# Performance work log

Hardware: AMD Instinct MI355X
Metric: run time of the kernel (lower is better)

Reference implementation:

```python
import jax, jax.numpy as jnp
import numpy as np

EPS = 1e-5
HEADS = 4
C = 128
GROUPS = 32  # min(32, 128//4)
SR = 2
SCALE = (C // HEADS) ** -0.5


def group_norm(x, gamma, beta, groups=GROUPS, eps=EPS):
    N, Ch, H, W = x.shape
    xg = x.reshape(N, groups, Ch // groups, H, W)
    mu = xg.mean(axis=(2, 3, 4), keepdims=True)
    var = xg.var(axis=(2, 3, 4), keepdims=True)
    xg = (xg - mu) * jax.lax.rsqrt(var + eps)
    x = xg.reshape(N, Ch, H, W)
    return x * gamma[None, :, None, None] + beta[None, :, None, None]


def conv1x1(x, W, b):
    # x: [N,C,H,W], W: [Cout,Cin], b: [Cout]
    return jnp.einsum('nchw,oc->nohw', x, W) + b[None, :, None, None]


def avg_pool2(x):
    N, Ch, H, W = x.shape
    return x.reshape(N, Ch, H // SR, SR, W // SR, SR).mean(axis=(3, 5))


def to_heads(x):
    # [N,C,H,W] -> [N,h,HW,C//h]  (matches view(N,h,C/h,HW).permute(0,1,3,2))
    N, Ch, H, W = x.shape
    return x.reshape(N, HEADS, Ch // HEADS, H * W).transpose(0, 1, 3, 2)


def setup_inputs() -> dict:
    key = jax.random.key(0)
    ks = jax.random.split(key, 16)
    B, H, W = 8, 64, 64
    s = 1.0 / np.sqrt(C)
    inp = {
        'q_src': jax.random.normal(ks[0], (B, C, H, W), jnp.float32),
        'k_src': jax.random.normal(ks[1], (B, C, H, W), jnp.float32),
        'v_src': jax.random.normal(ks[2], (B, C, H, W), jnp.float32),
        'Wq': jax.random.normal(ks[3], (C, C), jnp.float32) * s,
        'bq': jnp.zeros((C,), jnp.float32),
        'Wk': jax.random.normal(ks[4], (C, C), jnp.float32) * s,
        'bk': jnp.zeros((C,), jnp.float32),
        'Wv': jax.random.normal(ks[5], (C, C), jnp.float32) * s,
        'bv': jnp.zeros((C,), jnp.float32),
        'Wp': jax.random.normal(ks[6], (C, C), jnp.float32) * s,
        'bp': jnp.zeros((C,), jnp.float32),
        'g_nq': jnp.ones((C,), jnp.float32), 'b_nq': jnp.zeros((C,), jnp.float32),
        'g_nk': jnp.ones((C,), jnp.float32), 'b_nk': jnp.zeros((C,), jnp.float32),
        'g_nv': jnp.ones((C,), jnp.float32), 'b_nv': jnp.zeros((C,), jnp.float32),
        'g_srk': jnp.ones((C,), jnp.float32), 'b_srk': jnp.zeros((C,), jnp.float32),
        'g_srv': jnp.ones((C,), jnp.float32), 'b_srv': jnp.zeros((C,), jnp.float32),
    }
    return inp


def reference(q_src, k_src, v_src, Wq, bq, Wk, bk, Wv, bv, Wp, bp,
              g_nq, b_nq, g_nk, b_nk, g_nv, b_nv, g_srk, b_srk, g_srv, b_srv):
    # Q path: GN -> 1x1 conv
    q = conv1x1(group_norm(q_src, g_nq, b_nq), Wq, bq)
    # K/V paths: SR (avgpool + GN) -> GN -> 1x1 conv
    k = conv1x1(group_norm(group_norm(avg_pool2(k_src), g_srk, b_srk), g_nk, b_nk), Wk, bk)
    v = conv1x1(group_norm(group_norm(avg_pool2(v_src), g_srv, b_srv), g_nv, b_nv), Wv, bv)

    N, Cq, Hq, Wq_ = q.shape
    qh, kh, vh = to_heads(q), to_heads(k), to_heads(v)  # [N,h,L,d]
    attn = jnp.einsum('nhqd,nhkd->nhqk', qh * SCALE, kh)  # [N,h,Lq,Lk]
    attn = jax.nn.softmax(attn, axis=-1)
    out = jnp.einsum('nhqk,nhkd->nhqd', attn, vh)  # [N,h,Lq,d]
    out = out.transpose(0, 1, 3, 2).reshape(N, Cq, Hq, Wq_)
    return conv1x1(out, Wp, bp)
```

## Files before the change

### kernel.cpp

```cpp
#include <hip/hip_runtime.h>

typedef __attribute__((ext_vector_type(8)))  short s8v;
typedef __attribute__((ext_vector_type(4)))  short s4v;
typedef __attribute__((ext_vector_type(16))) float f16v;
typedef __attribute__((ext_vector_type(2)))  int   i2v;
typedef __attribute__((ext_vector_type(2)))  float f2v;

__device__ __forceinline__ unsigned short f2bf(float f) {
  union { float f; unsigned u; } v; v.f = f;
  unsigned r = v.u + 0x7FFFu + ((v.u >> 16) & 1u);
  return (unsigned short)(r >> 16);
}
__device__ __forceinline__ float bf2f(unsigned short b) {
  return __uint_as_float((unsigned)b << 16);
}
__device__ __forceinline__ float fexp2(float x) {
#if __has_builtin(__builtin_amdgcn_exp2f)
  return __builtin_amdgcn_exp2f(x);
#else
  return exp2f(x);
#endif
}
__device__ __forceinline__ f2v mk2(float a, float b) { f2v r; r[0] = a; r[1] = b; return r; }

__device__ __forceinline__ void gn_stats_body(
    int blk, const float* __restrict__ x, const float* __restrict__ gamma,
    const float* __restrict__ beta, float* __restrict__ ab, float* sh)
{
  int n = blk >> 5, g = blk & 31;
  int t = threadIdx.x; int cl = t >> 6, lane = t & 63;
  const float4* x4 = (const float4*)(x + (size_t)(n * 128 + g * 4 + cl) * 4096);
  float s = 0.f, ss = 0.f;
  #pragma unroll
  for (int j = 0; j < 16; ++j) {
    float4 v = x4[lane + 64 * j];
    s  += v.x + v.y + v.z + v.w;
    ss += v.x * v.x + v.y * v.y + v.z * v.z + v.w * v.w;
  }
  #pragma unroll
  for (int m = 32; m >= 1; m >>= 1) { s += __shfl_xor(s, m); ss += __shfl_xor(ss, m); }
  if (lane == 0) { sh[cl] = s; sh[4 + cl] = ss; }
  __syncthreads();
  if (t < 4) {
    float mu = (sh[0] + sh[1] + sh[2] + sh[3]) * (1.f / 16384.f);
    float e  = (sh[4] + sh[5] + sh[6] + sh[7]) * (1.f / 16384.f);
    float r  = rsqrtf(e - mu * mu + 1e-5f);
    int c = g * 4 + t;
    float al = gamma[c] * r;
    ab[n * 128 + c] = al;
    ab[1024 + n * 128 + c] = beta[c] - mu * al;
  }
}

__device__ __forceinline__ void pool_aff_body(
    int blk, const float* __restrict__ x,
    const float* __restrict__ g1, const float* __restrict__ b1,
    const float* __restrict__ g2, const float* __restrict__ b2,
    float* __restrict__ pooled, float* __restrict__ ab, float* sh)
{
  int n = blk >> 5, g = blk & 31;
  int t = threadIdx.x; int cl = t >> 6, lane = t & 63;
  int c = g * 4 + cl;
  const float* xb = x + (size_t)(n * 128 + c) * 4096;
  float* pb = pooled + (size_t)(n * 128 + c) * 1024;
  float s = 0.f, ss = 0.f;
  #pragma unroll
  for (int j = 0; j < 8; ++j) {
    int pp = (lane + 64 * j) * 2;
    int py = pp >> 5, px2 = pp & 31;
    const float* r0 = xb + py * 128 + px2 * 2;
    float4 A = *(const float4*)r0;
    float4 B = *(const float4*)(r0 + 64);
    float v0 = 0.25f * (A.x + A.y + B.x + B.y);
    float v1 = 0.25f * (A.z + A.w + B.z + B.w);
    float2 wv; wv.x = v0; wv.y = v1;
    *(float2*)(pb + pp) = wv;
    s += v0 + v1; ss += v0 * v0 + v1 * v1;
  }
  #pragma unroll
  for (int m = 32; m >= 1; m >>= 1) { s += __shfl_xor(s, m); ss += __shfl_xor(ss, m); }
  if (lane == 0) { sh[cl] = s; sh[4 + cl] = ss; }
  __syncthreads();
  if (t < 4) {
    float mu1 = (sh[0] + sh[1] + sh[2] + sh[3]) * (1.f / 4096.f);
    float e1  = (sh[4] + sh[5] + sh[6] + sh[7]) * (1.f / 4096.f);
    float r1  = rsqrtf(e1 - mu1 * mu1 + 1e-5f);
    float mzs = 0.f, e2s = 0.f;
    #pragma unroll
    for (int cc = 0; cc < 4; ++cc) {
      int ch = g * 4 + cc;
      float a = r1 * g1[ch];
      float d = b1[ch] - mu1 * a;
      float m = sh[cc] * (1.f / 1024.f);
      float q = sh[4 + cc] * (1.f / 1024.f);
      mzs += a * m + d;
      e2s += a * a * q + 2.f * a * d * m + d * d;
    }
    float mu2 = 0.25f * mzs;
    float r2  = rsqrtf(0.25f * e2s - mu2 * mu2 + 1e-5f);
    int ch = g * 4 + t;
    float a = r1 * g1[ch];
    float d = b1[ch] - mu1 * a;
    ab[n * 128 + ch] = a * r2 * g2[ch];
    ab[1024 + n * 128 + ch] = (d - mu2) * r2 * g2[ch] + b2[ch];
  }
}

__device__ __forceinline__ void wsplit_body(
    int b, const float* __restrict__ W, unsigned short* __restrict__ whi,
    unsigned short* __restrict__ wlo)
{
  int idx = b * 256 + threadIdx.x;
  #pragma unroll
  for (int k = 0; k < 4; ++k) {
    int f = idx + k * 4096;
    int o = f >> 7, c = f & 127;
    float v = W[f];
    unsigned short hb = f2bf(v);
    unsigned short lb = f2bf(v - bf2f(hb));
    int cq = c >> 2;
    int adr = (o * 16 + ((cq >> 1) ^ (o & 7))) * 8 + (cq & 1) * 4 + (c & 3);
    whi[adr] = hb; wlo[adr] = lb;
  }
}

__global__ __launch_bounds__(256) void prep_k(
    const float* __restrict__ q_src, const float* __restrict__ g_nq, const float* __restrict__ b_nq,
    const float* __restrict__ k_src, const float* __restrict__ g_srk, const float* __restrict__ b_srk,
    const float* __restrict__ g_nk, const float* __restrict__ b_nk,
    const float* __restrict__ v_src, const float* __restrict__ g_srv, const float* __restrict__ b_srv,
    const float* __restrict__ g_nv, const float* __restrict__ b_nv,
    const float* __restrict__ Wp,
    float* __restrict__ qab, float* __restrict__ kab, float* __restrict__ vab,
    float* __restrict__ knp, float* __restrict__ vnp,
    unsigned short* __restrict__ whi, unsigned short* __restrict__ wlo)
{
  __shared__ float sh[8];
  int b = blockIdx.x;
  if (b < 256) gn_stats_body(b, q_src, g_nq, b_nq, qab, sh);
  else if (b < 512) pool_aff_body(b - 256, k_src, g_srk, b_srk, g_nk, b_nk, knp, kab, sh);
  else if (b < 768) pool_aff_body(b - 512, v_src, g_srv, b_srv, g_nv, b_nv, vnp, vab, sh);
  else wsplit_body(b - 768, Wp, whi, wlo);
}

__device__ __forceinline__ void conv_body(
    int blk, const float* __restrict__ x, const float* __restrict__ ab,
    const float* __restrict__ W, const float* __restrict__ bias,
    unsigned short* __restrict__ po, int S, float outScale, int vt_mode,
    unsigned short* smem)
{
  unsigned short* Wsw = smem;
  unsigned short* xsw = smem + 16384;
  int t = threadIdx.x;
  int spb = S >> 7;
  int n  = blk / spb;
  int s0 = (blk % spb) << 7;

  #pragma unroll
  for (int k = 0; k < 16; ++k) {
    int f4 = t + (k << 8);
    int o = f4 >> 5, cq = f4 & 31;
    float4 wq = *(const float4*)(W + (size_t)o * 128 + cq * 4);
    union { unsigned q[2]; s4v v; } hv;
    asm("v_cvt_pk_bf16_f32 %0, %1, %2" : "=v"(hv.q[0]) : "v"(wq.x), "v"(wq.y));
    asm("v_cvt_pk_bf16_f32 %0, %1, %2" : "=v"(hv.q[1]) : "v"(wq.z), "v"(wq.w));
    *(s4v*)(Wsw + (o * 16 + ((cq >> 1) ^ (o & 7))) * 8 + (cq & 1) * 4) = hv.v;
  }
  int sl = t & 127, coh = t >> 7;
  for (int co = coh; co < 16; co += 2) {
    const float* xb = x + (size_t)(n * 128 + co * 8) * S + s0 + sl;
    const float* aa = ab + n * 128 + co * 8;
    const float* bb = aa + 1024;
    float f[8];
    #pragma unroll
    for (int e = 0; e < 8; ++e) f[e] = fmaf(xb[(size_t)e * S], aa[e], bb[e]);
    union { unsigned q[4]; s8v v; } xv;
    #pragma unroll
    for (int e = 0; e < 4; ++e)
      asm("v_cvt_pk_bf16_f32 %0, %1, %2" : "=v"(xv.q[e]) : "v"(f[2*e]), "v"(f[2*e+1]));
    *(s8v*)(xsw + (co * 128 + sl) * 8) = xv.v;
  }
  __syncthreads();

  int lane = t & 63, w = t >> 6;
  int l31 = lane & 31, h = lane >> 5;
  int wo = (w & 1) << 6, wsp = (w >> 1) << 6;
  f16v acc00 = {}, acc01 = {}, acc10 = {}, acc11 = {};
  #pragma unroll
  for (int reg = 0; reg < 16; ++reg) {
    int rm = (reg & 3) + ((reg >> 2) << 3) + (h << 2);
    float b0 = bias[wo + rm], b1 = bias[wo + 32 + rm];
    acc00[reg] = b0; acc01[reg] = b0; acc10[reg] = b1; acc11[reg] = b1;
  }
  const s8v* Wv = (const s8v*)Wsw;
  const s8v* Xv = (const s8v*)xsw;
  int o0 = wo + l31, o1 = wo + 32 + l31;
  #pragma unroll
  for (int cs = 0; cs < 8; ++cs) {
    int kk = cs * 2 + h;
    s8v a0 = Wv[o0 * 16 + (kk ^ (o0 & 7))];
    s8v a1 = Wv[o1 * 16 + (kk ^ (o1 & 7))];
    s8v b0 = Xv[kk * 128 + wsp + l31];
    s8v b1 = Xv[kk * 128 + wsp + 32 + l31];
    acc00 = __builtin_amdgcn_mfma_f32_32x32x16_bf16(a0, b0, acc00, 0, 0, 0);
    acc01 = __builtin_amdgcn_mfma_f32_32x32x16_bf16(a0, b1, acc01, 0, 0, 0);
    acc10 = __builtin_amdgcn_mfma_f32_32x32x16_bf16(a1, b0, acc10, 0, 0, 0);
    acc11 = __builtin_amdgcn_mfma_f32_32x32x16_bf16(a1, b1, acc11, 0, 0, 0);
  }
  __syncthreads();
  unsigned short* ot = smem;
  #pragma unroll
  for (int reg = 0; reg < 16; ++reg) {
    int rm = (reg & 3) + ((reg >> 2) << 3) + (h << 2);
    ot[(wo + rm) * 132 + wsp + l31]           = f2bf(acc00[reg] * outScale);
    ot[(wo + rm) * 132 + wsp + 32 + l31]      = f2bf(acc01[reg] * outScale);
    ot[(wo + 32 + rm) * 132 + wsp + l31]      = f2bf(acc10[reg] * outScale);
    ot[(wo + 32 + rm) * 132 + wsp + 32 + l31] = f2bf(acc11[reg] * outScale);
  }
  __syncthreads();
  if (!vt_mode) {
    int d = t & 31;
    for (int i = 0; i < 64; ++i) {
      int idx2 = (t >> 5) + (i << 3);
      int s = idx2 & 127, ohi_ = idx2 >> 7;
      po[((size_t)(n * 4 + ohi_) * S + s0 + s) * 32 + d] = ot[(ohi_ * 32 + d) * 132 + s];
    }
  } else {
    int s = t & 127;
    for (int i = 0; i < 64; ++i) {
      int rr = (t >> 7) + i * 2;
      po[((size_t)(n * 4 + (rr >> 5)) * 32 + (rr & 31)) * S + s0 + s] = ot[rr * 132 + s];
    }
  }
}

__global__ __launch_bounds__(256) void convs_k(
    const float* __restrict__ q_src, const float* __restrict__ qab,
    const float* __restrict__ Wq, const float* __restrict__ bq, unsigned short* __restrict__ qhb,
    const float* __restrict__ knp, const float* __restrict__ kab,
    const float* __restrict__ Wk, const float* __restrict__ bk, unsigned short* __restrict__ khb,
    const float* __restrict__ vnp, const float* __restrict__ vab,
    const float* __restrict__ Wv, const float* __restrict__ bv, unsigned short* __restrict__ vtb,
    float qscale)
{
  __shared__ __align__(16) unsigned short smem[32768];
  int b = blockIdx.x;
  if (b < 256)      conv_body(b,       q_src, qab, Wq, bq, qhb, 4096, qscale, 0, smem);
  else if (b < 320) conv_body(b - 256, knp,   kab, Wk, bk, khb, 1024, 1.0f,   0, smem);
  else              conv_body(b - 320, vnp,   vab, Wv, bv, vtb, 1024, 1.0f,   1, smem);
}

__global__ __launch_bounds__(256) void conv_hilo_k(
    const float* __restrict__ xo, const unsigned short* __restrict__ whi,
    const unsigned short* __restrict__ wlo, const float* __restrict__ bias,
    float* __restrict__ out)
{
  __shared__ __align__(16) unsigned short Xh[4096], Xl[4096];
  int t = threadIdx.x;
  int lane = t & 63, w = t >> 6;
  int l31 = lane & 31, h = lane >> 5;
  int n = blockIdx.x >> 7, s0 = (blockIdx.x & 127) << 5;

  int ol = w * 32 + l31;
  const s8v* WH = (const s8v*)whi;
  const s8v* WL = (const s8v*)wlo;
  s8v ah[8], al[8];
  #pragma unroll
  for (int cs = 0; cs < 8; ++cs) {
    int kk = cs * 2 + h;
    int ia = ol * 16 + (kk ^ (ol & 7));
    ah[cs] = WH[ia];
    al[cs] = WL[ia];
  }

  #pragma unroll
  for (int i = 0; i < 2; ++i) {
    int co = t & 15, sl = (t >> 4) + i * 16;
    const float* xp = xo + (((size_t)(n * 4096 + s0 + sl)) << 7) + co * 8;
    float4 A = *(const float4*)xp;
    float4 B = *(const float4*)(xp + 4);
    float f[8] = {A.x, A.y, A.z, A.w, B.x, B.y, B.z, B.w};
    union { unsigned q[4]; s8v v; } H, L;
    #pragma unroll
    for (int e = 0; e < 4; ++e) {
      unsigned hp;
      asm("v_cvt_pk_bf16_f32 %0, %1, %2" : "=v"(hp) : "v"(f[2*e]), "v"(f[2*e+1]));
      H.q[e] = hp;
      float h0 = __uint_as_float(hp << 16);
      float h1 = __uint_as_float(hp & 0xFFFF0000u);
      float l0 = f[2*e] - h0, l1 = f[2*e+1] - h1;
      asm("v_cvt_pk_bf16_f32 %0, %1, %2" : "=v"(L.q[e]) : "v"(l0), "v"(l1));
    }
    int dst = ((co * 32 + sl) * 8) ^ ((co & 7) << 3);
    *(s8v*)(Xh + dst) = H.v;
    *(s8v*)(Xl + dst) = L.v;
  }
  __syncthreads();

  f16v acc;
  #pragma unroll
  for (int reg = 0; reg < 16; ++reg) {
    int rm = (reg & 3) + ((reg >> 2) << 3) + (h << 2);
    acc[reg] = bias[w * 32 + rm];
  }
  #pragma unroll
  for (int cs = 0; cs < 8; ++cs) {
    int kk = cs * 2 + h;
    int ix = ((kk * 32 + l31) * 8) ^ ((kk & 7) << 3);
    s8v bh = *(const s8v*)(Xh + ix);
    s8v bl = *(const s8v*)(Xl + ix);
    acc = __builtin_amdgcn_mfma_f32_32x32x16_bf16(ah[cs], bh, acc, 0, 0, 0);
    acc = __builtin_amdgcn_mfma_f32_32x32x16_bf16(ah[cs], bl, acc, 0, 0, 0);
    acc = __builtin_amdgcn_mfma_f32_32x32x16_bf16(al[cs], bh, acc, 0, 0, 0);
  }
  #pragma unroll
  for (int reg = 0; reg < 16; ++reg) {
    int rm = (reg & 3) + ((reg >> 2) << 3) + (h << 2);
    out[(size_t)(n * 128 + w * 32 + rm) * 4096 + s0 + l31] = acc[reg];
  }
}

__global__ __launch_bounds__(256, 4) void attn_k(
    const unsigned short* __restrict__ qh, const unsigned short* __restrict__ kh,
    const unsigned short* __restrict__ vt, float* __restrict__ obuf)
{
  __shared__ __align__(16) unsigned short Klds[2][2048];
  __shared__ __align__(16) unsigned short Vlds[2][2048];
  __shared__ float linv[128];
  int t = threadIdx.x;
  int lane = t & 63, w = t >> 6;
  int l31 = lane & 31, h = lane >> 5;
  int blk = blockIdx.x;
  int nh = blk & 31, qb = blk >> 5;

  const unsigned short* qp = qh + (((size_t)nh * 4096 + qb * 128 + w * 32 + l31) << 5);
  s8v qf0 = *(const s8v*)(qp + h * 8);
  s8v qf1 = *(const s8v*)(qp + (2 + h) * 8);

  size_t kvb = (size_t)nh << 15;
  const unsigned short* kg = kh + kvb + ((t >> 2) << 5) + ((t & 3) << 3);
  const unsigned short* vg = vt + kvb + ((size_t)(t >> 3) << 10) + ((t & 7) << 3);
  int ku = ((t >> 2) << 2) + ((t & 3) ^ ((t >> 3) & 3));
  int vu = ((t >> 3) << 3) + ((t & 7) ^ ((t >> 3) & 7));

  s8v rk = *(const s8v*)kg;
  s8v rv = *(const s8v*)vg;
  *(s8v*)&Klds[0][ku * 8] = rk;
  *(s8v*)&Vlds[0][vu * 8] = rv;

  const f16v fz = {};
  f16v oacc = fz;
  f2v lp0 = mk2(0.f, 0.f), lp1 = mk2(0.f, 0.f);
  int kx = (l31 >> 1) & 3;
  int vx = l31 & 7;

  #pragma unroll 2
  for (int tile = 0; tile < 16; ++tile) {
    int buf = tile & 1;
    __syncthreads();
    if (tile < 15) {
      int j0 = (tile + 1) << 6;
      rk = *(const s8v*)(kg + (size_t)j0 * 32);
      rv = *(const s8v*)(vg + j0);
    }
    const unsigned short* Kb = Klds[buf];
    const unsigned short* Vb = Vlds[buf];
    #pragma unroll
    for (int s = 0; s < 2; ++s) {
      int rb = s * 128 + l31 * 4;
      s8v kf0 = *(const s8v*)(Kb + ((rb + (h ^ kx)) << 3));
      s8v kf1 = *(const s8v*)(Kb + ((rb + ((2 + h) ^ kx)) << 3));
      __builtin_amdgcn_s_setprio(1);
      f16v sf = __builtin_amdgcn_mfma_f32_32x32x16_bf16(kf0, qf0, fz, 0, 0, 0);
      sf = __builtin_amdgcn_mfma_f32_32x32x16_bf16(kf1, qf1, sf, 0, 0, 0);
      __builtin_amdgcn_s_setprio(0);
      float p[16];
      #pragma unroll
      for (int r = 0; r < 16; ++r) p[r] = fexp2(sf[r]);
      lp0 += mk2(p[0], p[1]);  lp1 += mk2(p[2], p[3]);
      lp0 += mk2(p[4], p[5]);  lp1 += mk2(p[6], p[7]);
      lp0 += mk2(p[8], p[9]);  lp1 += mk2(p[10], p[11]);
      lp0 += mk2(p[12], p[13]); lp1 += mk2(p[14], p[15]);
      unsigned c[8];
      #pragma unroll
      for (int q = 0; q < 8; ++q)
        asm("v_cvt_pk_bf16_f32 %0, %1, %2" : "=v"(c[q]) : "v"(p[2 * q]), "v"(p[2 * q + 1]));
      i2v s02 = __builtin_amdgcn_permlane32_swap((int)c[0], (int)c[2], false, false);
      i2v s13 = __builtin_amdgcn_permlane32_swap((int)c[1], (int)c[3], false, false);
      i2v s46 = __builtin_amdgcn_permlane32_swap((int)c[4], (int)c[6], false, false);
      i2v s57 = __builtin_amdgcn_permlane32_swap((int)c[5], (int)c[7], false, false);
      union { int u[4]; s8v v; } u0, u1;
      u0.u[0] = s02[0]; u0.u[1] = s13[0]; u0.u[2] = s02[1]; u0.u[3] = s13[1];
      u1.u[0] = s46[0]; u1.u[1] = s57[0]; u1.u[2] = s46[1]; u1.u[3] = s57[1];
      s8v vf0 = *(const s8v*)(Vb + ((l31 * 8 + ((s * 4 + h) ^ vx)) << 3));
      s8v vf1 = *(const s8v*)(Vb + ((l31 * 8 + ((s * 4 + 2 + h) ^ vx)) << 3));
      __builtin_amdgcn_s_setprio(1);
      oacc = __builtin_amdgcn_mfma_f32_32x32x16_bf16(u0.v, vf0, oacc, 0, 0, 0);
      oacc = __builtin_amdgcn_mfma_f32_32x32x16_bf16(u1.v, vf1, oacc, 0, 0, 0);
      __builtin_amdgcn_s_setprio(0);
    }
    if (tile < 15) {
      *(s8v*)&Klds[buf ^ 1][ku * 8] = rk;
      *(s8v*)&Vlds[buf ^ 1][vu * 8] = rv;
    }
  }

  float l_part = lp0[0] + lp0[1] + lp1[0] + lp1[1];
  float l_tot = l_part + __shfl_xor(l_part, 32);
  if (h == 0) linv[w * 32 + l31] = 1.0f / l_tot;
  __syncthreads();
  int n = nh >> 2, hh = nh & 3;
  size_t obase = (((size_t)n * 4096 + qb * 128) << 7) + hh * 32 + l31;
  #pragma unroll
  for (int reg = 0; reg < 16; ++reg) {
    int rm = (reg & 3) + ((reg >> 2) << 3) + (h << 2);
    obuf[obase + ((size_t)(w * 32 + rm) << 7)] = oacc[reg] * linv[w * 32 + rm];
  }
}

extern "C" void kernel_launch(void* const* d_in, const int* in_sizes, int n_in,
                              void* d_out, int out_size, void* d_ws, size_t ws_size,
                              hipStream_t stream)
{
  (void)in_sizes; (void)n_in; (void)out_size; (void)ws_size;
  const float* q_src = (const float*)d_in[0];
  const float* k_src = (const float*)d_in[1];
  const float* v_src = (const float*)d_in[2];
  const float* Wq = (const float*)d_in[3];
  const float* bq = (const float*)d_in[4];
  const float* Wk = (const float*)d_in[5];
  const float* bk = (const float*)d_in[6];
  const float* Wv = (const float*)d_in[7];
  const float* bv = (const float*)d_in[8];
  const float* Wp = (const float*)d_in[9];
  const float* bp = (const float*)d_in[10];
  const float* g_nq  = (const float*)d_in[11];
  const float* b_nq  = (const float*)d_in[12];
  const float* g_nk  = (const float*)d_in[13];
  const float* b_nk  = (const float*)d_in[14];
  const float* g_nv  = (const float*)d_in[15];
  const float* b_nv  = (const float*)d_in[16];
  const float* g_srk = (const float*)d_in[17];
  const float* b_srk = (const float*)d_in[18];
  const float* g_srv = (const float*)d_in[19];
  const float* b_srv = (const float*)d_in[20];

  unsigned short* qhb = (unsigned short*)d_ws;
  unsigned short* khb = qhb + 4194304;
  unsigned short* vtb = khb + 1048576;
  float* obuf = (float*)(vtb + 1048576);
  float* knp  = obuf + 4194304;
  float* vnp  = knp + 1048576;
  float* qab  = vnp + 1048576;
  float* kab  = qab + 2048;
  float* vab  = kab + 2048;
  unsigned short* whi = (unsigned short*)(vab + 2048);
  unsigned short* wlo = whi + 16384;

  const float QSCALE = 0.17677669529663688f * 1.44269504088896340f;

  prep_k<<<784, 256, 0, stream>>>(q_src, g_nq, b_nq,
                                  k_src, g_srk, b_srk, g_nk, b_nk,
                                  v_src, g_srv, b_srv, g_nv, b_nv,
                                  Wp, qab, kab, vab, knp, vnp, whi, wlo);
  convs_k<<<384, 256, 0, stream>>>(q_src, qab, Wq, bq, qhb,
                                   knp, kab, Wk, bk, khb,
                                   vnp, vab, Wv, bv, vtb, QSCALE);
  attn_k<<<1024, 256, 0, stream>>>(qhb, khb, vtb, obuf);
  conv_hilo_k<<<1024, 256, 0, stream>>>(obuf, whi, wlo, bp, (float*)d_out);
}
```

Before: 70.42 us.

## Double KV tile size in attention and pack conv output stores to 32-bit

The attention kernel now stages 128 keys/values per tile instead of 64. That halves the number of loop iterations and block barriers and doubles the loads in flight per prefetch. The PV product is split across two independent accumulators, which shortens the MFMA dependency chain, and the two are summed at the end. The conv epilogue now writes packed 32-bit pairs instead of 16-bit stores to cut global store transactions. In exchange, LDS use per block doubles and register pressure rises, which could limit occupancy under launch_bounds(256,4).

```diff
diff --git a/kernel.cpp b/kernel.cpp
--- a/kernel.cpp
+++ b/kernel.cpp
@@ -219,17 +219,23 @@
   }
   __syncthreads();
   if (!vt_mode) {
-    int d = t & 31;
-    for (int i = 0; i < 64; ++i) {
-      int idx2 = (t >> 5) + (i << 3);
-      int s = idx2 & 127, ohi_ = idx2 >> 7;
-      po[((size_t)(n * 4 + ohi_) * S + s0 + s) * 32 + d] = ot[(ohi_ * 32 + d) * 132 + s];
+    unsigned* po32 = (unsigned*)po;
+    int d2 = t & 15;
+    for (int i = 0; i < 32; ++i) {
+      int pr = (t >> 4) + (i << 4);
+      int s = pr & 127, ohi_ = pr >> 7;
+      unsigned lo = ot[(ohi_ * 32 + d2 * 2) * 132 + s];
+      unsigned hi = ot[(ohi_ * 32 + d2 * 2 + 1) * 132 + s];
+      po32[((size_t)(n * 4 + ohi_) * S + s0 + s) * 16 + d2] = lo | (hi << 16);
     }
   } else {
-    int s = t & 127;
-    for (int i = 0; i < 64; ++i) {
-      int rr = (t >> 7) + i * 2;
-      po[((size_t)(n * 4 + (rr >> 5)) * 32 + (rr & 31)) * S + s0 + s] = ot[rr * 132 + s];
+    unsigned* po32 = (unsigned*)po;
+    const unsigned* ot32 = (const unsigned*)ot;
+    int sp = t & 63;
+    for (int i = 0; i < 32; ++i) {
+      int rr = (t >> 6) + (i << 2);
+      po32[((size_t)(n * 4 + (rr >> 5)) * 32 + (rr & 31)) * (S >> 1) + (s0 >> 1) + sp] =
+          ot32[rr * 66 + sp];
     }
   }
 }
@@ -324,8 +330,8 @@
     const unsigned short* __restrict__ qh, const unsigned short* __restrict__ kh,
     const unsigned short* __restrict__ vt, float* __restrict__ obuf)
 {
-  __shared__ __align__(16) unsigned short Klds[2][2048];
-  __shared__ __align__(16) unsigned short Vlds[2][2048];
+  __shared__ __align__(16) unsigned short Klds[2][4096];
+  __shared__ __align__(16) unsigned short Vlds[2][4096];
   __shared__ float linv[128];
   int t = threadIdx.x;
   int lane = t & 63, w = t >> 6;
@@ -339,35 +345,40 @@
 
   size_t kvb = (size_t)nh << 15;
   const unsigned short* kg = kh + kvb + ((t >> 2) << 5) + ((t & 3) << 3);
-  const unsigned short* vg = vt + kvb + ((size_t)(t >> 3) << 10) + ((t & 7) << 3);
+  const unsigned short* vg = vt + kvb + ((size_t)(t >> 4) << 10) + ((t & 15) << 3);
   int ku = ((t >> 2) << 2) + ((t & 3) ^ ((t >> 3) & 3));
-  int vu = ((t >> 3) << 3) + ((t & 7) ^ ((t >> 3) & 7));
-
-  s8v rk = *(const s8v*)kg;
-  s8v rv = *(const s8v*)vg;
-  *(s8v*)&Klds[0][ku * 8] = rk;
-  *(s8v*)&Vlds[0][vu * 8] = rv;
+  int vu = ((t >> 4) << 4) + ((t & 15) ^ ((t >> 4) & 15));
+
+  s8v rk0 = *(const s8v*)kg;
+  s8v rk1 = *(const s8v*)(kg + 2048);
+  s8v rv0 = *(const s8v*)vg;
+  s8v rv1 = *(const s8v*)(vg + 16384);
+  *(s8v*)&Klds[0][ku * 8]        = rk0;
+  *(s8v*)&Klds[0][ku * 8 + 2048] = rk1;
+  *(s8v*)&Vlds[0][vu * 8]        = rv0;
+  *(s8v*)&Vlds[0][vu * 8 + 2048] = rv1;
 
   const f16v fz = {};
-  f16v oacc = fz;
+  f16v oa0 = fz, oa1 = fz;
   f2v lp0 = mk2(0.f, 0.f), lp1 = mk2(0.f, 0.f);
   int kx = (l31 >> 1) & 3;
-  int vx = l31 & 7;
-
-  #pragma unroll 2
-  for (int tile = 0; tile < 16; ++tile) {
+  int vx = l31 & 15;
+
+  for (int tile = 0; tile < 8; ++tile) {
     int buf = tile & 1;
     __syncthreads();
-    if (tile < 15) {
-      int j0 = (tile + 1) << 6;
-      rk = *(const s8v*)(kg + (size_t)j0 * 32);
-      rv = *(const s8v*)(vg + j0);
+    if (tile < 7) {
+      int j0 = (tile + 1) << 7;
+      rk0 = *(const s8v*)(kg + (size_t)j0 * 32);
+      rk1 = *(const s8v*)(kg + (size_t)j0 * 32 + 2048);
+      rv0 = *(const s8v*)(vg + j0);
+      rv1 = *(const s8v*)(vg + j0 + 16384);
     }
     const unsigned short* Kb = Klds[buf];
     const unsigned short* Vb = Vlds[buf];
     #pragma unroll
-    for (int s = 0; s < 2; ++s) {
-      int rb = s * 128 + l31 * 4;
+    for (int s2 = 0; s2 < 4; ++s2) {
+      int rb = s2 * 128 + l31 * 4;
       s8v kf0 = *(const s8v*)(Kb + ((rb + (h ^ kx)) << 3));
       s8v kf1 = *(const s8v*)(Kb + ((rb + ((2 + h) ^ kx)) << 3));
       __builtin_amdgcn_s_setprio(1);
@@ -392,19 +403,27 @@
       union { int u[4]; s8v v; } u0, u1;
       u0.u[0] = s02[0]; u0.u[1] = s13[0]; u0.u[2] = s02[1]; u0.u[3] = s13[1];
       u1.u[0] = s46[0]; u1.u[1] = s57[0]; u1.u[2] = s46[1]; u1.u[3] = s57[1];
-      s8v vf0 = *(const s8v*)(Vb + ((l31 * 8 + ((s * 4 + h) ^ vx)) << 3));
-      s8v vf1 = *(const s8v*)(Vb + ((l31 * 8 + ((s * 4 + 2 + h) ^ vx)) << 3));
+      s8v vf0 = *(const s8v*)(Vb + ((l31 * 16 + ((s2 * 4 + h) ^ vx)) << 3));
+      s8v vf1 = *(const s8v*)(Vb + ((l31 * 16 + ((s2 * 4 + 2 + h) ^ vx)) << 3));
       __builtin_amdgcn_s_setprio(1);
-      oacc = __builtin_amdgcn_mfma_f32_32x32x16_bf16(u0.v, vf0, oacc, 0, 0, 0);
-      oacc = __builtin_amdgcn_mfma_f32_32x32x16_bf16(u1.v, vf1, oacc, 0, 0, 0);
+      if (s2 & 1) {
+        oa1 = __builtin_amdgcn_mfma_f32_32x32x16_bf16(u0.v, vf0, oa1, 0, 0, 0);
+        oa1 = __builtin_amdgcn_mfma_f32_32x32x16_bf16(u1.v, vf1, oa1, 0, 0, 0);
+      } else {
+        oa0 = __builtin_amdgcn_mfma_f32_32x32x16_bf16(u0.v, vf0, oa0, 0, 0, 0);
+        oa0 = __builtin_amdgcn_mfma_f32_32x32x16_bf16(u1.v, vf1, oa0, 0, 0, 0);
+      }
       __builtin_amdgcn_s_setprio(0);
     }
-    if (tile < 15) {
-      *(s8v*)&Klds[buf ^ 1][ku * 8] = rk;
-      *(s8v*)&Vlds[buf ^ 1][vu * 8] = rv;
-    }
-  }
-
+    if (tile < 7) {
+      *(s8v*)&Klds[buf ^ 1][ku * 8]        = rk0;
+      *(s8v*)&Klds[buf ^ 1][ku * 8 + 2048] = rk1;
+      *(s8v*)&Vlds[buf ^ 1][vu * 8]        = rv0;
+      *(s8v*)&Vlds[buf ^ 1][vu * 8 + 2048] = rv1;
+    }
+  }
+
+  f16v oacc = oa0 + oa1;
   float l_part = lp0[0] + lp0[1] + lp1[0] + lp1[1];
   float l_tot = l_part + __shfl_xor(l_part, 32);
   if (h == 0) linv[w * 32 + l31] = 1.0f / l_tot;
```

Result: faster. 66.42 us (-5.7%).

## Fuse attention with output projection and widen conv epilogue stores to 32-bit

Applied to the files above, without the earlier changes.

Merges the attention kernel and the hi/lo bf16 output-projection kernel into one 1024-thread block that computes all four heads for a 128-query tile. The normalized attention output is split into hi/lo bf16 in shared memory and fed straight into the projection MFMAs, so the fp32 intermediate buffer no longer makes a round trip through global memory and one launch is dropped. The conv epilogue stores now pack two bf16 values per 32-bit write. The trade-offs are fewer, larger blocks (256 blocks of 1024 threads), about 66KB of LDS per block, and no explicit unroll on the tile loop, all of which can lower occupancy.

```diff
diff --git a/kernel.cpp b/kernel.cpp
--- a/kernel.cpp
+++ b/kernel.cpp
@@ -219,17 +219,23 @@
   }
   __syncthreads();
   if (!vt_mode) {
-    int d = t & 31;
-    for (int i = 0; i < 64; ++i) {
-      int idx2 = (t >> 5) + (i << 3);
-      int s = idx2 & 127, ohi_ = idx2 >> 7;
-      po[((size_t)(n * 4 + ohi_) * S + s0 + s) * 32 + d] = ot[(ohi_ * 32 + d) * 132 + s];
+    unsigned* po32 = (unsigned*)po;
+    int d2 = t & 15;
+    for (int i = 0; i < 32; ++i) {
+      int pr = (t >> 4) + (i << 4);
+      int s = pr & 127, ohi_ = pr >> 7;
+      unsigned lo = ot[(ohi_ * 32 + d2 * 2) * 132 + s];
+      unsigned hi = ot[(ohi_ * 32 + d2 * 2 + 1) * 132 + s];
+      po32[((size_t)(n * 4 + ohi_) * S + s0 + s) * 16 + d2] = lo | (hi << 16);
     }
   } else {
-    int s = t & 127;
-    for (int i = 0; i < 64; ++i) {
-      int rr = (t >> 7) + i * 2;
-      po[((size_t)(n * 4 + (rr >> 5)) * 32 + (rr & 31)) * S + s0 + s] = ot[rr * 132 + s];
+    unsigned* po32 = (unsigned*)po;
+    const unsigned* ot32 = (const unsigned*)ot;
+    int sp = t & 63;
+    for (int i = 0; i < 32; ++i) {
+      int rr = (t >> 6) + (i << 2);
+      po32[((size_t)(n * 4 + (rr >> 5)) * 32 + (rr & 31)) * (S >> 1) + (s0 >> 1) + sp] =
+          ot32[rr * 66 + sp];
     }
   }
 }
@@ -250,103 +256,38 @@
   else              conv_body(b - 320, vnp,   vab, Wv, bv, vtb, 1024, 1.0f,   1, smem);
 }
 
-__global__ __launch_bounds__(256) void conv_hilo_k(
-    const float* __restrict__ xo, const unsigned short* __restrict__ whi,
-    const unsigned short* __restrict__ wlo, const float* __restrict__ bias,
+__global__ __launch_bounds__(1024) void attn_proj_k(
+    const unsigned short* __restrict__ qh, const unsigned short* __restrict__ kh,
+    const unsigned short* __restrict__ vt, const unsigned short* __restrict__ whi,
+    const unsigned short* __restrict__ wlo, const float* __restrict__ bp,
     float* __restrict__ out)
 {
-  __shared__ __align__(16) unsigned short Xh[4096], Xl[4096];
+  __shared__ __align__(16) unsigned char SM[67584];
+  unsigned short* S16 = (unsigned short*)SM;
+  float* linvp = (float*)(SM + 65536);
   int t = threadIdx.x;
   int lane = t & 63, w = t >> 6;
   int l31 = lane & 31, h = lane >> 5;
-  int n = blockIdx.x >> 7, s0 = (blockIdx.x & 127) << 5;
-
-  int ol = w * 32 + l31;
-  const s8v* WH = (const s8v*)whi;
-  const s8v* WL = (const s8v*)wlo;
-  s8v ah[8], al[8];
-  #pragma unroll
-  for (int cs = 0; cs < 8; ++cs) {
-    int kk = cs * 2 + h;
-    int ia = ol * 16 + (kk ^ (ol & 7));
-    ah[cs] = WH[ia];
-    al[cs] = WL[ia];
-  }
-
-  #pragma unroll
-  for (int i = 0; i < 2; ++i) {
-    int co = t & 15, sl = (t >> 4) + i * 16;
-    const float* xp = xo + (((size_t)(n * 4096 + s0 + sl)) << 7) + co * 8;
-    float4 A = *(const float4*)xp;
-    float4 B = *(const float4*)(xp + 4);
-    float f[8] = {A.x, A.y, A.z, A.w, B.x, B.y, B.z, B.w};
-    union { unsigned q[4]; s8v v; } H, L;
-    #pragma unroll
-    for (int e = 0; e < 4; ++e) {
-      unsigned hp;
-      asm("v_cvt_pk_bf16_f32 %0, %1, %2" : "=v"(hp) : "v"(f[2*e]), "v"(f[2*e+1]));
-      H.q[e] = hp;
-      float h0 = __uint_as_float(hp << 16);
-      float h1 = __uint_as_float(hp & 0xFFFF0000u);
-      float l0 = f[2*e] - h0, l1 = f[2*e+1] - h1;
-      asm("v_cvt_pk_bf16_f32 %0, %1, %2" : "=v"(L.q[e]) : "v"(l0), "v"(l1));
-    }
-    int dst = ((co * 32 + sl) * 8) ^ ((co & 7) << 3);
-    *(s8v*)(Xh + dst) = H.v;
-    *(s8v*)(Xl + dst) = L.v;
-  }
-  __syncthreads();
-
-  f16v acc;
-  #pragma unroll
-  for (int reg = 0; reg < 16; ++reg) {
-    int rm = (reg & 3) + ((reg >> 2) << 3) + (h << 2);
-    acc[reg] = bias[w * 32 + rm];
-  }
-  #pragma unroll
-  for (int cs = 0; cs < 8; ++cs) {
-    int kk = cs * 2 + h;
-    int ix = ((kk * 32 + l31) * 8) ^ ((kk & 7) << 3);
-    s8v bh = *(const s8v*)(Xh + ix);
-    s8v bl = *(const s8v*)(Xl + ix);
-    acc = __builtin_amdgcn_mfma_f32_32x32x16_bf16(ah[cs], bh, acc, 0, 0, 0);
-    acc = __builtin_amdgcn_mfma_f32_32x32x16_bf16(ah[cs], bl, acc, 0, 0, 0);
-    acc = __builtin_amdgcn_mfma_f32_32x32x16_bf16(al[cs], bh, acc, 0, 0, 0);
-  }
-  #pragma unroll
-  for (int reg = 0; reg < 16; ++reg) {
-    int rm = (reg & 3) + ((reg >> 2) << 3) + (h << 2);
-    out[(size_t)(n * 128 + w * 32 + rm) * 4096 + s0 + l31] = acc[reg];
-  }
-}
-
-__global__ __launch_bounds__(256, 4) void attn_k(
-    const unsigned short* __restrict__ qh, const unsigned short* __restrict__ kh,
-    const unsigned short* __restrict__ vt, float* __restrict__ obuf)
-{
-  __shared__ __align__(16) unsigned short Klds[2][2048];
-  __shared__ __align__(16) unsigned short Vlds[2][2048];
-  __shared__ float linv[128];
-  int t = threadIdx.x;
-  int lane = t & 63, w = t >> 6;
-  int l31 = lane & 31, h = lane >> 5;
+  int hh = w & 3, qr = w >> 2;
   int blk = blockIdx.x;
-  int nh = blk & 31, qb = blk >> 5;
-
-  const unsigned short* qp = qh + (((size_t)nh * 4096 + qb * 128 + w * 32 + l31) << 5);
+  int n = blk >> 5, qb = blk & 31;
+
+  const unsigned short* qp =
+      qh + (((size_t)(n * 4 + hh) * 4096 + qb * 128 + qr * 32 + l31) << 5);
   s8v qf0 = *(const s8v*)(qp + h * 8);
   s8v qf1 = *(const s8v*)(qp + (2 + h) * 8);
 
-  size_t kvb = (size_t)nh << 15;
-  const unsigned short* kg = kh + kvb + ((t >> 2) << 5) + ((t & 3) << 3);
-  const unsigned short* vg = vt + kvb + ((size_t)(t >> 3) << 10) + ((t & 7) << 3);
-  int ku = ((t >> 2) << 2) + ((t & 3) ^ ((t >> 3) & 3));
-  int vu = ((t >> 3) << 3) + ((t & 7) ^ ((t >> 3) & 7));
+  int sh_ = t >> 8, si = t & 255;
+  size_t kvb = (size_t)(n * 4 + sh_) << 15;
+  const unsigned short* kg = kh + kvb + ((si >> 2) << 5) + ((si & 3) << 3);
+  const unsigned short* vg = vt + kvb + ((size_t)(si >> 3) << 10) + ((si & 7) << 3);
+  int ku = (si & ~3) | ((si & 3) ^ ((si >> 3) & 3));
+  int vu = (si & ~7) | ((si & 7) ^ ((si >> 3) & 7));
 
   s8v rk = *(const s8v*)kg;
-  s8v rv = *(const s8v*)vg;
-  *(s8v*)&Klds[0][ku * 8] = rk;
-  *(s8v*)&Vlds[0][vu * 8] = rv;
+  s8v rvv = *(const s8v*)vg;
+  *(s8v*)(S16 + sh_ * 2048 + ku * 8) = rk;
+  *(s8v*)(S16 + 16384 + sh_ * 2048 + vu * 8) = rvv;
 
   const f16v fz = {};
   f16v oacc = fz;
@@ -354,17 +295,16 @@
   int kx = (l31 >> 1) & 3;
   int vx = l31 & 7;
 
-  #pragma unroll 2
   for (int tile = 0; tile < 16; ++tile) {
     int buf = tile & 1;
     __syncthreads();
     if (tile < 15) {
-      int j0 = (tile + 1) << 6;
-      rk = *(const s8v*)(kg + (size_t)j0 * 32);
-      rv = *(const s8v*)(vg + j0);
-    }
-    const unsigned short* Kb = Klds[buf];
-    const unsigned short* Vb = Vlds[buf];
+      int j = (tile + 1) << 6;
+      rk = *(const s8v*)(kg + (size_t)j * 32);
+      rvv = *(const s8v*)(vg + j);
+    }
+    const unsigned short* Kb = S16 + (buf * 4 + hh) * 2048;
+    const unsigned short* Vb = S16 + 16384 + (buf * 4 + hh) * 2048;
     #pragma unroll
     for (int s = 0; s < 2; ++s) {
       int rb = s * 128 + l31 * 4;
@@ -400,21 +340,64 @@
       __builtin_amdgcn_s_setprio(0);
     }
     if (tile < 15) {
-      *(s8v*)&Klds[buf ^ 1][ku * 8] = rk;
-      *(s8v*)&Vlds[buf ^ 1][vu * 8] = rv;
+      *(s8v*)(S16 + ((buf ^ 1) * 4 + sh_) * 2048 + ku * 8) = rk;
+      *(s8v*)(S16 + 16384 + ((buf ^ 1) * 4 + sh_) * 2048 + vu * 8) = rvv;
     }
   }
 
   float l_part = lp0[0] + lp0[1] + lp1[0] + lp1[1];
   float l_tot = l_part + __shfl_xor(l_part, 32);
-  if (h == 0) linv[w * 32 + l31] = 1.0f / l_tot;
-  __syncthreads();
-  int n = nh >> 2, hh = nh & 3;
-  size_t obase = (((size_t)n * 4096 + qb * 128) << 7) + hh * 32 + l31;
+  if (h == 0) linvp[hh * 128 + qr * 32 + l31] = 1.0f / l_tot;
+  __syncthreads();
+
+  unsigned short* Xh16 = S16;
+  unsigned short* Xl16 = S16 + 16384;
+  int ch = hh * 32 + l31, co = ch >> 3, el = ch & 7;
   #pragma unroll
   for (int reg = 0; reg < 16; ++reg) {
     int rm = (reg & 3) + ((reg >> 2) << 3) + (h << 2);
-    obuf[obase + ((size_t)(w * 32 + rm) << 7)] = oacc[reg] * linv[w * 32 + rm];
+    int row = qr * 32 + rm;
+    float val = oacc[reg] * linvp[hh * 128 + row];
+    unsigned short hb = f2bf(val);
+    unsigned short lb = f2bf(val - bf2f(hb));
+    int xu = co * 128 + (row ^ co);
+    Xh16[xu * 8 + el] = hb;
+    Xl16[xu * 8 + el] = lb;
+  }
+  __syncthreads();
+
+  int ol = hh * 32 + l31;
+  const s8v* WH = (const s8v*)whi;
+  const s8v* WL = (const s8v*)wlo;
+  s8v ah[8], al[8];
+  #pragma unroll
+  for (int cs = 0; cs < 8; ++cs) {
+    int kk = cs * 2 + h;
+    int ia = ol * 16 + (kk ^ (ol & 7));
+    ah[cs] = WH[ia];
+    al[cs] = WL[ia];
+  }
+  f16v acc;
+  #pragma unroll
+  for (int reg = 0; reg < 16; ++reg) {
+    int rm = (reg & 3) + ((reg >> 2) << 3) + (h << 2);
+    acc[reg] = bp[hh * 32 + rm];
+  }
+  int srow = qr * 32 + l31;
+  #pragma unroll
+  for (int cs = 0; cs < 8; ++cs) {
+    int kk = cs * 2 + h;
+    int xu = kk * 128 + (srow ^ kk);
+    s8v bh = *(const s8v*)(Xh16 + xu * 8);
+    s8v bl = *(const s8v*)(Xl16 + xu * 8);
+    acc = __builtin_amdgcn_mfma_f32_32x32x16_bf16(ah[cs], bh, acc, 0, 0, 0);
+    acc = __builtin_amdgcn_mfma_f32_32x32x16_bf16(ah[cs], bl, acc, 0, 0, 0);
+    acc = __builtin_amdgcn_mfma_f32_32x32x16_bf16(al[cs], bh, acc, 0, 0, 0);
+  }
+  #pragma unroll
+  for (int reg = 0; reg < 16; ++reg) {
+    int rm = (reg & 3) + ((reg >> 2) << 3) + (h << 2);
+    out[(size_t)(n * 128 + hh * 32 + rm) * 4096 + qb * 128 + srow] = acc[reg];
   }
 }
 
@@ -448,8 +431,7 @@
   unsigned short* qhb = (unsigned short*)d_ws;
   unsigned short* khb = qhb + 4194304;
   unsigned short* vtb = khb + 1048576;
-  float* obuf = (float*)(vtb + 1048576);
-  float* knp  = obuf + 4194304;
+  float* knp  = (float*)(vtb + 1048576);
   float* vnp  = knp + 1048576;
   float* qab  = vnp + 1048576;
   float* kab  = qab + 2048;
@@ -466,6 +448,5 @@
   convs_k<<<384, 256, 0, stream>>>(q_src, qab, Wq, bq, qhb,
                                    knp, kab, Wk, bk, khb,
                                    vnp, vab, Wv, bv, vtb, QSCALE);
-  attn_k<<<1024, 256, 0, stream>>>(qhb, khb, vtb, obuf);
-  conv_hilo_k<<<1024, 256, 0, stream>>>(obuf, whi, wlo, bp, (float*)d_out);
-}
+  attn_proj_k<<<256, 1024, 0, stream>>>(qhb, khb, vtb, whi, wlo, bp, (float*)d_out);
+}
```

Result: faster. 63.08 us (median of 2 runs) (-10.4%).
